# Performance work log

Hardware: AMD Instinct MI355X
Metric: run time of the kernel (lower is better)

## Reference

```python
import jax, jax.numpy as jnp
import numpy as np

B, T, D, H, DK, DV, FF = 4, 1024, 1024, 16, 64, 64, 4096


def setup_inputs() -> dict:
    key = jax.random.key(0)
    ks = jax.random.split(key, 16)
    sc = 0.02  # init scale (original uses uninitialized torch.empty; use small randn)
    n = lambda k, shape: jax.random.normal(k, shape, jnp.float32) * sc
    return dict(
        x=jax.random.normal(ks[0], (B, T, D), jnp.float32),
        y=jax.random.normal(ks[1], (B, T, D), jnp.float32),
        Wq1=n(ks[2], (H, D, DK)), Wk1=n(ks[3], (H, D, DK)),
        Wv1=n(ks[4], (H, D, DV)), Wo1=n(ks[5], (D, D)),
        Wq2=n(ks[6], (H, D, DK)), Wk2=n(ks[7], (H, D, DK)),
        Wv2=n(ks[8], (H, D, DV)), Wo2=n(ks[9], (D, D)),
        W_in=n(ks[10], (FF, D)), b_in=jnp.zeros((FF,), jnp.float32),
        W_out=n(ks[11], (D, FF)), b_out=jnp.zeros((D,), jnp.float32),
    )


def _mha(q, k, v, Wq, Wk, Wv, Wo):
    # per-head projections: (B,T,D) x (H,D,dk) -> (B,H,T,dk)
    WQ = jnp.einsum('btd,hdk->bhtk', q, Wq)
    WK = jnp.einsum('bsd,hdk->bhsk', k, Wk)
    WV = jnp.einsum('bsd,hdv->bhsv', v, Wv)
    scores = jnp.einsum('bhtk,bhsk->bhts', WQ, WK) / jnp.sqrt(jnp.float32(DK))
    # NOTE: original code softmaxes over dim=2 (the QUERY axis), kept faithfully
    attn = jax.nn.softmax(scores, axis=2)
    partial = jnp.einsum('bhts,bhsv->bhtv', attn, WV)
    partial = partial.transpose(0, 2, 1, 3).reshape(q.shape[0], q.shape[1], -1)  # (B,T,H*dv)
    return partial @ Wo


def _sub_norm(o):
    mean = o.mean(-1, keepdims=True)
    std = o.std(-1, ddof=1, keepdims=True)  # torch.std default is unbiased
    return o - mean - std  # faithful: subtract (not divide by) std


def reference(x, y, Wq1, Wk1, Wv1, Wo1, Wq2, Wk2, Wv2, Wo2, W_in, b_in, W_out, b_out):
    out1 = _sub_norm(_mha(y, y, y, Wq1, Wk1, Wv1, Wo1) + y)
    out2 = _sub_norm(_mha(y, x, x, Wq2, Wk2, Wv2, Wo2) + out1)
    ff = jax.nn.relu(y @ W_in.T + b_in) @ W_out.T + b_out  # FFN applied to y, as in source
    return _sub_norm(ff + out2)
```

## Files before the change

### kernel.cpp

```cpp
#include <hip/hip_runtime.h>


typedef unsigned short u16;
typedef __bf16 bf16x8 __attribute__((ext_vector_type(8)));
typedef float f32x4 __attribute__((ext_vector_type(4)));

__device__ __forceinline__ u16 f2bf(float f) {
    unsigned int u = __float_as_uint(f);
    u += 0x7fffu + ((u >> 16) & 1u);
    return (u16)(u >> 16);
}
__device__ __forceinline__ float bf2f(u16 b) {
    return __uint_as_float(((unsigned int)b) << 16);
}

typedef __attribute__((address_space(1))) const void* as1cv;
typedef __attribute__((address_space(3))) void* as3v;
__device__ __forceinline__ void gl_lds16(const void* g, void* l) {
    __builtin_amdgcn_global_load_lds((as1cv)g, (as3v)l, 16, 0, 0);
}

__global__ __launch_bounds__(256) void mega_pack_k(
    const float* __restrict__ yf, u16* __restrict__ yb,
    const float* __restrict__ xf, u16* __restrict__ xb,
    const float* __restrict__ W_in, u16* __restrict__ Winb,
    const float* __restrict__ W_out, u16* __restrict__ Woutb,
    const float* __restrict__ Wq1, const float* __restrict__ Wk1,
    const float* __restrict__ Wv1, const float* __restrict__ Wq2,
    u16* __restrict__ W1cat,
    const float* __restrict__ Wk2, const float* __restrict__ Wv2,
    u16* __restrict__ Wkv2t,
    const float* __restrict__ Wo1, u16* __restrict__ Wo1t,
    const float* __restrict__ Wo2, u16* __restrict__ Wo2t,
    float* __restrict__ csumz)
{
    __shared__ float tile[64][65];
    int id = blockIdx.x;
    if (id >= 18432) {
        long i = (long)(id - 18432) * 256 + threadIdx.x;
        float4 zz; zz.x = 0.f; zz.y = 0.f; zz.z = 0.f; zz.w = 0.f;
        reinterpret_cast<float4*>(csumz)[i] = zz;
        return;
    }
    if (id < 16384) {
        int j = id >> 12, local = id & 4095;
        const float* in; u16* out;
        switch (j) {
            case 0:  in = yf;    out = yb;    break;
            case 1:  in = xf;    out = xb;    break;
            case 2:  in = W_in;  out = Winb;  break;
            default: in = W_out; out = Woutb; break;
        }
        long i = (long)local * 256 + threadIdx.x;
        float4 v = reinterpret_cast<const float4*>(in)[i];
        ushort4 o;
        o.x = f2bf(v.x); o.y = f2bf(v.y); o.z = f2bf(v.z); o.w = f2bf(v.w);
        reinterpret_cast<ushort4*>(out)[i] = o;
        return;
    }
    int t = id - 16384;
    int pj = t >> 8, local = t & 255;
    const float* in; u16* out;
    int Q, R, bx, by, bz;
    if (pj < 6) {
        switch (pj) {
            case 0:  in = Wq1; out = W1cat;           break;
            case 1:  in = Wk1; out = W1cat + 1048576; break;
            case 2:  in = Wv1; out = W1cat + 2097152; break;
            case 3:  in = Wq2; out = W1cat + 3145728; break;
            case 4:  in = Wk2; out = Wkv2t;           break;
            default: in = Wv2; out = Wkv2t + 1048576; break;
        }
        Q = 1024; R = 64; bx = 0; by = local & 15; bz = local >> 4;
    } else {
        in = (pj == 6) ? Wo1 : Wo2; out = (pj == 6) ? Wo1t : Wo2t;
        Q = 1024; R = 1024; bx = local & 15; by = local >> 4; bz = 0;
    }
    int r0 = bx * 64, q0 = by * 64;
    int tx = threadIdx.x & 63, ty = threadIdx.x >> 6;
    const float* inp = in + ((long)bz * Q + q0) * R + r0;
    #pragma unroll
    for (int i = 0; i < 64; i += 4)
        tile[ty + i][tx] = inp[(long)(ty + i) * R + tx];
    __syncthreads();
    u16* outp = out + ((long)bz * R + r0) * Q + q0;
    #pragma unroll
    for (int i = 0; i < 64; i += 4)
        outp[(long)(ty + i) * Q + tx] = f2bf(tile[tx][ty + i]);
}

__global__ __launch_bounds__(256) void tscale2_k(
    const u16* __restrict__ in1, long ld1, long zs1,
    const u16* __restrict__ in2, long ld2, long zs2,
    u16* __restrict__ Vt, const float* __restrict__ csum) {
    __shared__ u16 tile[64][66];
    int z = blockIdx.z;
    int m = z >> 2, zb = z & 3;
    const u16* in; long ld, zs;
    if (m) { in = in2; ld = ld2; zs = zs2; } else { in = in1; ld = ld1; zs = zs1; }
    const u16* inz = in + (long)zb * zs;
    u16* outz = Vt + (long)m * 4194304 + (long)zb * 1048576;
    const float* cs = csum + m * 65536 + (long)zb * 16384;
    int r0 = blockIdx.y * 64;
    int c0 = blockIdx.x * 64;
    int tx = threadIdx.x & 63, ty = threadIdx.x >> 6;
    #pragma unroll
    for (int i = 0; i < 64; i += 4)
        tile[ty + i][tx] = inz[(long)(r0 + ty + i) * ld + c0 + tx];
    __syncthreads();
    #pragma unroll
    for (int i = 0; i < 64; i += 4) {
        int orow = c0 + ty + i;
        float f = bf2f(tile[tx][ty + i]) / cs[(orow >> 6) * 1024 + r0 + tx];
        outz[(long)orow * 1024 + r0 + tx] = f2bf(f);
    }
}

template<int BM, int BN, int BK, int WM, int WN, int OUT_BF16, int EPI, int SWZ, int KS, int MRG>
__global__ __launch_bounds__(256) void gemm_k(
    const u16* __restrict__ A, long lda, long a_zin, long a_zout,
    const u16* __restrict__ B, long ldb, long b_zin, long b_zout,
    void* __restrict__ Cv, long ldc, long c_zin, long c_zout,
    int zin, int K, float alpha, const float* __restrict__ bias,
    float* __restrict__ csum,
    const u16* __restrict__ A2, long lda2,
    const u16* __restrict__ B2, long ldb2, long b_zout2,
    float* __restrict__ csum2)
{
    static_assert(BK == 64, "staging assumes BK=64");
    constexpr int WTM = BM / WM;
    constexpr int WTN = BN / WN;
    constexpr int TM = WTM / 16;
    constexpr int TN = WTN / 16;
    __shared__ __align__(16) u16 smem[(BM + BN) * BK];
    u16* As = smem;
    u16* Bs = smem + BM * BK;

    int bx, by, z;
    if (SWZ == 4) {
        int L = blockIdx.x;
        if (KS > 1) { z = L >> 9; L &= 511; } else { z = 0; }
        by = (L & 7) * 4 + ((L >> 3) & 3);
        bx = L >> 5;
    } else {
        bx = blockIdx.x; by = blockIdx.y; z = blockIdx.z;
    }
    if (MRG) {
        int m2 = z >> 6; z &= 63;
        if (m2) { A = A2; lda = lda2; B = B2; ldb = ldb2; b_zout = b_zout2; csum = csum2; }
    }
    int zi = z % zin, zo = z / zin;
    A += (long)zi * a_zin + (long)zo * a_zout;
    B += (long)zi * b_zin + (long)zo * b_zout;
    long coff = (long)zi * c_zin + (long)zo * c_zout;

    int tid = threadIdx.x;
    int lane = tid & 63;
    int wave = tid >> 6;
    int wm = wave / WN, wn = wave % WN;
    long bm0 = (long)by * BM, bn0 = (long)bx * BN;

    f32x4 acc[TM][TN];
    #pragma unroll
    for (int i = 0; i < TM; ++i)
        #pragma unroll
        for (int j = 0; j < TN; ++j) {
            acc[i][j][0] = 0.f; acc[i][j][1] = 0.f;
            acc[i][j][2] = 0.f; acc[i][j][3] = 0.f;
        }

    int r16 = lane & 15;
    int quad = lane >> 4;
    int l8 = lane >> 3;
    int gsw = ((lane & 7) ^ l8) * 8;

    constexpr int ASTR = BM / 8;
    constexpr int BSTR = BN / 8;

    for (int k0 = 0; k0 < K; k0 += BK) {
        #pragma unroll
        for (int s = wave; s < ASTR; s += 4)
            gl_lds16(&A[(bm0 + s * 8 + l8) * lda + k0 + gsw], &As[s * 512]);
        #pragma unroll
        for (int s = wave; s < BSTR; s += 4)
            gl_lds16(&B[(bn0 + s * 8 + l8) * ldb + k0 + gsw], &Bs[s * 512]);
        __syncthreads();
        #pragma unroll
        for (int kk = 0; kk < BK; kk += 32) {
            int cb = (kk >> 3) + quad;
            bf16x8 av[TM], bv[TN];
            #pragma unroll
            for (int i = 0; i < TM; ++i) {
                int r = wm * WTM + i * 16 + r16;
                av[i] = *reinterpret_cast<const bf16x8*>(&As[r * 64 + ((cb ^ (r & 7)) * 8)]);
            }
            #pragma unroll
            for (int j = 0; j < TN; ++j) {
                int r = wn * WTN + j * 16 + r16;
                bv[j] = *reinterpret_cast<const bf16x8*>(&Bs[r * 64 + ((cb ^ (r & 7)) * 8)]);
            }
            #pragma unroll
            for (int i = 0; i < TM; ++i)
                #pragma unroll
                for (int j = 0; j < TN; ++j)
                    acc[i][j] = __builtin_amdgcn_mfma_f32_16x16x32_bf16(av[i], bv[j], acc[i][j], 0, 0, 0);
        }
        __syncthreads();
    }

    int rb = quad * 4;

    if (EPI == 4) {
        float csl[TN];
        #pragma unroll
        for (int j = 0; j < TN; ++j) csl[j] = 0.f;
        #pragma unroll
        for (int i = 0; i < TM; ++i)
            #pragma unroll
            for (int j = 0; j < TN; ++j)
                #pragma unroll
                for (int r = 0; r < 4; ++r)
                    csl[j] += __expf(acc[i][j][r] * alpha);
        #pragma unroll
        for (int j = 0; j < TN; ++j) {
            float cs = csl[j];
            cs += __shfl_xor(cs, 16, 64);
            cs += __shfl_xor(cs, 32, 64);
            if (quad == 0) {
                long col = bn0 + wn * WTN + j * 16 + r16;
                atomicAdd(&csum[((long)zo * zin + zi) * 1024 + col], cs);
            }
        }
        return;
    }

    constexpr int EB = OUT_BF16 ? 2 : 4;
    constexpr int CH = 16 / EB;
    constexpr int STRIDE = BN + CH;
    constexpr int LDSB = (BM + BN) * BK * 2;
    constexpr int EPASS = (BM * STRIDE * EB > LDSB) ? 2 : 1;
    constexpr int RPP = BM / EPASS;
    static_assert(RPP * STRIDE * EB <= LDSB, "epilogue tile overflows LDS");
    static_assert(EPASS == 1 || (WM == 2 && WTM == RPP), "pass/wave row alignment");
    constexpr int CPR = BN / CH;
    constexpr int NCH = RPP * CPR / 256;
    static_assert(RPP * CPR % 256 == 0, "store mapping");

    float* Ef = reinterpret_cast<float*>(smem);
    char* Cb = reinterpret_cast<char*>(Cv);

    for (int pass = 0; pass < EPASS; ++pass) {
        int p0 = pass * RPP;
        __syncthreads();
        #pragma unroll
        for (int i = 0; i < TM; ++i) {
            #pragma unroll
            for (int j = 0; j < TN; ++j) {
                int lcol = wn * WTN + j * 16 + r16;
                float bsv = (EPI == 1 || EPI == 2) ? bias[bn0 + lcol] : 0.f;
                #pragma unroll
                for (int r = 0; r < 4; ++r) {
                    int lrow = wm * WTM + i * 16 + rb + r;
                    if ((unsigned)(lrow - p0) < (unsigned)RPP) {
                        float v = acc[i][j][r] * alpha;
                        if (EPI == 1) { v += bsv; v = v > 0.f ? v : 0.f; }
                        else if (EPI == 2) { v += bsv; }
                        if (OUT_BF16) smem[(lrow - p0) * STRIDE + lcol] = f2bf(v);
                        else          Ef[(lrow - p0) * STRIDE + lcol] = v;
                    }
                }
            }
        }
        __syncthreads();
        #pragma unroll
        for (int c = 0; c < NCH; ++c) {
            int cid = tid + c * 256;
            int row = cid / CPR, ch = cid - row * CPR;
            int4 v = *reinterpret_cast<const int4*>(
                reinterpret_cast<const char*>(smem) + (row * STRIDE + ch * CH) * EB);
            long gidx = coff + (bm0 + p0 + row) * ldc + bn0 + ch * CH;
            *reinterpret_cast<int4*>(Cb + gidx * EB) = v;
        }
    }
}


__device__ __forceinline__ void bar_raw() {
    asm volatile("" ::: "memory");
    __builtin_amdgcn_s_barrier();
    asm volatile("" ::: "memory");
}

template<int N> __device__ __forceinline__ void vmw() {
    if constexpr (N == 10) asm volatile("s_waitcnt vmcnt(10)" ::: "memory");
    else if constexpr (N == 8) asm volatile("s_waitcnt vmcnt(8)" ::: "memory");
    else if constexpr (N == 4) asm volatile("s_waitcnt vmcnt(4)" ::: "memory");
    else if constexpr (N == 2) asm volatile("s_waitcnt vmcnt(2)" ::: "memory");
    else if constexpr (N == 0) asm volatile("s_waitcnt vmcnt(0)" ::: "memory");
}

__device__ __forceinline__ void stage_half(const u16* __restrict__ base, long ld, int kt,
                                           u16* __restrict__ lds, int half, int wave) {
    const u16* src = base + (long)kt * 64;
    #pragma unroll
    for (int u = 0; u < 2; ++u) {
        int s = half * 16 + u * 8 + wave;
        gl_lds16(src + (long)(s * 8) * ld, lds + s * 512);
    }
}

template<int IH>
__device__ __forceinline__ void read_a8(bf16x8 (&av)[4][2], const u16* __restrict__ As,
                                        int wm, int r16, int quad) {
    #pragma unroll
    for (int ii = 0; ii < 4; ++ii) {
        int r = IH * 128 + wm * 64 + ii * 16 + r16;
        #pragma unroll
        for (int kx = 0; kx < 2; ++kx)
            av[ii][kx] = *reinterpret_cast<const bf16x8*>(&As[r * 64 + (((kx * 4 + quad) ^ (r & 7)) * 8)]);
    }
}

template<int JH>
__device__ __forceinline__ void read_b8(bf16x8 (&bv)[2][2], const u16* __restrict__ Bs,
                                        int wn, int r16, int quad) {
    #pragma unroll
    for (int j = 0; j < 2; ++j) {
        int r = JH * 128 + wn * 32 + j * 16 + r16;
        #pragma unroll
        for (int kx = 0; kx < 2; ++kx)
            bv[j][kx] = *reinterpret_cast<const bf16x8*>(&Bs[r * 64 + (((kx * 4 + quad) ^ (r & 7)) * 8)]);
    }
}

template<int IH, int JH>
__device__ __forceinline__ void mfma_q(f32x4 (&acc)[2][4][2][2],
                                       const bf16x8 (&av)[4][2], const bf16x8 (&bv)[2][2]) {
    #pragma unroll
    for (int kx = 0; kx < 2; ++kx)
        #pragma unroll
        for (int ii = 0; ii < 4; ++ii)
            #pragma unroll
            for (int j = 0; j < 2; ++j)
                acc[IH][ii][JH][j] = __builtin_amdgcn_mfma_f32_16x16x32_bf16(
                    av[ii][kx], bv[j][kx], acc[IH][ii][JH][j], 0, 0, 0);
}

template<int MODE>
__device__ __forceinline__ void tile_iter(
    int t, f32x4 (&acc)[2][4][2][2], bf16x8 (&av)[4][2], bf16x8 (&bvh)[2][2][2],
    u16* __restrict__ smem, const u16* __restrict__ Ab, long lda,
    const u16* __restrict__ Bb, long ldb, int wave, int wm, int wn, int r16, int quad)
{
    u16* As0 = smem + (t & 1) * 32768;
    u16* Bs0 = As0 + 16384;
    u16* As1 = smem + ((t + 1) & 1) * 32768;
    read_a8<0>(av, As0, wm, r16, quad);
    read_b8<0>(bvh[0], Bs0, wn, r16, quad);
    if (MODE < 2) stage_half(Ab, lda, t + 1, As1, 1, wave);
    vmw<MODE == 0 ? 10 : (MODE == 1 ? 10 : 2)>();
    bar_raw(); __builtin_amdgcn_sched_barrier(0);
    __builtin_amdgcn_s_setprio(1);
    mfma_q<0, 0>(acc, av, bvh[0]);
    __builtin_amdgcn_s_setprio(0);
    __builtin_amdgcn_sched_barrier(0);
    bar_raw();
    read_b8<1>(bvh[1], Bs0, wn, r16, quad);
    if (MODE == 0) stage_half(Ab, lda, t + 2, As0, 0, wave);
    vmw<MODE == 0 ? 10 : (MODE == 1 ? 8 : 0)>();
    bar_raw(); __builtin_amdgcn_sched_barrier(0);
    __builtin_amdgcn_s_setprio(1);
    mfma_q<0, 1>(acc, av, bvh[1]);
    __builtin_amdgcn_s_setprio(0);
    __builtin_amdgcn_sched_barrier(0);
    bar_raw();
    read_a8<1>(av, As0, wm, r16, quad);
    if (MODE == 0) stage_half(Bb, ldb, t + 2, Bs0, 0, wave);
    bar_raw(); __builtin_amdgcn_sched_barrier(0);
    __builtin_amdgcn_s_setprio(1);
    mfma_q<1, 0>(acc, av, bvh[0]);
    __builtin_amdgcn_s_setprio(0);
    __builtin_amdgcn_sched_barrier(0);
    bar_raw();
    if (MODE == 0) stage_half(Bb, ldb, t + 2, Bs0, 1, wave);
    if (MODE < 2) vmw<MODE == 0 ? 10 : 4>();
    bar_raw(); __builtin_amdgcn_sched_barrier(0);
    __builtin_amdgcn_s_setprio(1);
    mfma_q<1, 1>(acc, av, bvh[1]);
    __builtin_amdgcn_s_setprio(0);
    __builtin_amdgcn_sched_barrier(0);
    bar_raw();
}

template<int NT, int KS, int EPI, int OUT_BF16, int SPLITN>
__global__ __launch_bounds__(512, 2) void gemm8_k(
    const u16* __restrict__ A, long lda,
    const u16* __restrict__ B, long ldb,
    void* __restrict__ Cv, void* __restrict__ Cv2, long ldc,
    int K, float alpha, const float* __restrict__ bias, long czs)
{
    __shared__ __align__(16) u16 smem[65536];

    int L = blockIdx.x;
    int z = 0;
    if (KS > 1) { z = L / (16 * NT); L -= z * 16 * NT; }
    int by = (L & 7) * 2 + ((L >> 3) & 1);
    int bx = L >> 4;
    if (KS > 1) { A += (long)z * K; B += (long)z * K; }

    int tid = threadIdx.x;
    int lane = tid & 63, wave = tid >> 6;
    int wm = wave >> 2, wn = wave & 3;
    int r16 = lane & 15, quad = lane >> 4, l8 = lane >> 3;
    int gsw = ((lane & 7) ^ l8) * 8;
    long bm0 = (long)by * 256, bn0 = (long)bx * 256;
    const u16* Ab = A + (bm0 + l8) * lda + gsw;
    const u16* Bb = B + (bn0 + l8) * ldb + gsw;

    f32x4 acc[2][4][2][2];
    #pragma unroll
    for (int a0 = 0; a0 < 2; ++a0)
        #pragma unroll
        for (int a1 = 0; a1 < 4; ++a1)
            #pragma unroll
            for (int a2 = 0; a2 < 2; ++a2)
                #pragma unroll
                for (int a3 = 0; a3 < 2; ++a3) {
                    acc[a0][a1][a2][a3][0] = 0.f; acc[a0][a1][a2][a3][1] = 0.f;
                    acc[a0][a1][a2][a3][2] = 0.f; acc[a0][a1][a2][a3][3] = 0.f;
                }
    bf16x8 av[4][2];
    bf16x8 bvh[2][2][2];

    int T = K >> 6;

    stage_half(Ab, lda, 0, smem,         0, wave);
    stage_half(Bb, ldb, 0, smem + 16384, 0, wave);
    stage_half(Bb, ldb, 0, smem + 16384, 1, wave);
    stage_half(Ab, lda, 0, smem,         1, wave);
    stage_half(Ab, lda, 1, smem + 32768, 0, wave);
    stage_half(Bb, ldb, 1, smem + 49152, 0, wave);
    stage_half(Bb, ldb, 1, smem + 49152, 1, wave);
    vmw<10>();
    bar_raw();

    for (int t = 0; t < T - 2; ++t)
        tile_iter<0>(t, acc, av, bvh, smem, Ab, lda, Bb, ldb, wave, wm, wn, r16, quad);
    tile_iter<1>(T - 2, acc, av, bvh, smem, Ab, lda, Bb, ldb, wave, wm, wn, r16, quad);
    tile_iter<2>(T - 1, acc, av, bvh, smem, Ab, lda, Bb, ldb, wave, wm, wn, r16, quad);

    constexpr int EB = OUT_BF16 ? 2 : 4;
    constexpr int EPASS = OUT_BF16 ? 1 : 2;
    bool sec = SPLITN && (bx >= NT / 2);
    char* Cb;
    long bnc = bn0;
    if (SPLITN) {
        Cb = reinterpret_cast<char*>(sec ? Cv2 : Cv);
        if (sec) bnc = bn0 - (long)(NT / 2) * 256;
    } else {
        Cb = reinterpret_cast<char*>((KS > 1 && z >= 2) ? Cv2 : Cv);
        if (KS > 1) Cb += (long)(z & 1) * czs * EB;
    }
    bool do_bias = (EPI == 1) || sec;
    float bsv[2][2];
    if (do_bias) {
        #pragma unroll
        for (int jh = 0; jh < 2; ++jh)
            #pragma unroll
            for (int j = 0; j < 2; ++j)
                bsv[jh][j] = bias[bnc + jh * 128 + wn * 32 + j * 16 + r16];
    }
    u16* sm16 = smem;
    float* smf = reinterpret_cast<float*>(smem);
    #pragma unroll
    for (int pass = 0; pass < EPASS; ++pass) {
        bar_raw();
        #pragma unroll
        for (int ih = 0; ih < 2; ++ih) {
            if (EPASS == 2 && ih != pass) continue;
            #pragma unroll
            for (int ii = 0; ii < 4; ++ii)
                #pragma unroll
                for (int jh = 0; jh < 2; ++jh)
                    #pragma unroll
                    for (int j = 0; j < 2; ++j)
                        #pragma unroll
                        for (int r = 0; r < 4; ++r) {
                            int lrow = (EPASS == 2 ? 0 : ih * 128) + wm * 64 + ii * 16 + quad * 4 + r;
                            int lcol = jh * 128 + wn * 32 + j * 16 + r16;
                            float v = acc[ih][ii][jh][j][r] * alpha;
                            if (do_bias) { v += bsv[jh][j]; v = v > 0.f ? v : 0.f; }
                            int scol = lcol ^ ((lrow & 7) * 8);
                            if (OUT_BF16) sm16[lrow * 256 + scol] = f2bf(v);
                            else          smf[lrow * 256 + scol] = v;
                        }
        }
        bar_raw();
        constexpr int CH = 16 / EB;
        constexpr int CPR = 256 / CH;
        constexpr int NCH = (OUT_BF16 ? 256 : 128) * CPR / 512;
        #pragma unroll
        for (int c = 0; c < NCH; ++c) {
            int cid = tid + c * 512;
            int row = cid / CPR, ch = cid - row * CPR;
            int col = (ch * CH) ^ ((row & 7) * 8);
            int4 v = *reinterpret_cast<const int4*>(
                reinterpret_cast<const char*>(smem) + ((long)row * 256 + col) * EB);
            long grow = bm0 + pass * 128 + row;
            *reinterpret_cast<int4*>(Cb + (grow * ldc + bnc + ch * CH) * EB) = v;
        }
    }
}

template<int MRG>
__global__ __launch_bounds__(256) void attn_pv_k(
    const u16* __restrict__ Qg, long ldq, long qbz,
    const u16* __restrict__ Kg, long ldk, long kbz,
    const u16* __restrict__ Vg, u16* __restrict__ outg,
    const u16* __restrict__ Qg2,
    const u16* __restrict__ Kg2, long ldk2, long kbz2,
    const u16* __restrict__ Vg2, u16* __restrict__ outg2)
{
    __shared__ __align__(16) u16 Qs[128 * 64];
    __shared__ __align__(16) u16 Ks[2][64 * 64];
    __shared__ __align__(16) u16 Vs[2][64 * 64];
    __shared__ __align__(16) u16 Es[128 * 64];

    int L = blockIdx.x;
    if (MRG) {
        int m = L >> 9; L &= 511;
        if (m) { Qg = Qg2; Kg = Kg2; ldk = ldk2; kbz = kbz2; Vg = Vg2; outg = outg2; }
    }
    int h  = (L & 7) * 2 + ((L >> 3) & 1);
    int tb = (L >> 4) & 7;
    int b  = L >> 7;

    const u16* Q  = Qg + (long)b * qbz + h * 64;
    const u16* Kp = Kg + (long)b * kbz + h * 64;
    const u16* Vp = Vg + (long)b * 1048576 + (long)h * 65536;
    u16* outp = outg + (long)b * 1048576 + (long)tb * 131072 + h * 64;

    int tid = threadIdx.x, lane = tid & 63, wave = tid >> 6;
    int wm = wave >> 1, wn = wave & 1;
    int r16 = lane & 15, quad = lane >> 4, l8 = lane >> 3;
    int gsw = ((lane & 7) ^ l8) * 8;
    long t0 = (long)tb * 128;

    #pragma unroll
    for (int s = wave; s < 16; s += 4)
        gl_lds16(&Q[(t0 + s * 8 + l8) * ldq + gsw], &Qs[s * 512]);
    #pragma unroll
    for (int s = wave; s < 8; s += 4) {
        gl_lds16(&Kp[(long)(s * 8 + l8) * ldk + gsw], &Ks[0][s * 512]);
        gl_lds16(&Vp[(long)(s * 8 + l8) * 1024 + gsw], &Vs[0][s * 512]);
    }

    f32x4 acc[4][2];
    #pragma unroll
    for (int i = 0; i < 4; ++i)
        #pragma unroll
        for (int j = 0; j < 2; ++j) {
            acc[i][j][0] = 0.f; acc[i][j][1] = 0.f;
            acc[i][j][2] = 0.f; acc[i][j][3] = 0.f;
        }

    for (int sc = 0; sc < 16; ++sc) {
        const u16* Ksc = Ks[sc & 1];
        const u16* Vsc = Vs[sc & 1];
        if (sc < 15) {
            int nc = sc + 1;
            u16* Kn = Ks[nc & 1];
            u16* Vn = Vs[nc & 1];
            #pragma unroll
            for (int s = wave; s < 8; s += 4) {
                gl_lds16(&Kp[(long)(nc * 64 + s * 8 + l8) * ldk + gsw], &Kn[s * 512]);
                gl_lds16(&Vp[(long)(s * 8 + l8) * 1024 + nc * 64 + gsw], &Vn[s * 512]);
            }
            asm volatile("s_waitcnt vmcnt(4)" ::: "memory");
        } else {
            asm volatile("s_waitcnt vmcnt(0)" ::: "memory");
        }
        bar_raw();

        f32x4 e[4][2];
        #pragma unroll
        for (int i = 0; i < 4; ++i)
            #pragma unroll
            for (int j = 0; j < 2; ++j) {
                e[i][j][0] = 0.f; e[i][j][1] = 0.f;
                e[i][j][2] = 0.f; e[i][j][3] = 0.f;
            }
        #pragma unroll
        for (int kk = 0; kk < 64; kk += 32) {
            int cb = (kk >> 3) + quad;
            bf16x8 av[4], bv[2];
            #pragma unroll
            for (int i = 0; i < 4; ++i) {
                int r = wm * 64 + i * 16 + r16;
                av[i] = *reinterpret_cast<const bf16x8*>(&Qs[r * 64 + ((cb ^ (r & 7)) * 8)]);
            }
            #pragma unroll
            for (int j = 0; j < 2; ++j) {
                int r = wn * 32 + j * 16 + r16;
                bv[j] = *reinterpret_cast<const bf16x8*>(&Ksc[r * 64 + ((cb ^ (r & 7)) * 8)]);
            }
            #pragma unroll
            for (int i = 0; i < 4; ++i)
                #pragma unroll
                for (int j = 0; j < 2; ++j)
                    e[i][j] = __builtin_amdgcn_mfma_f32_16x16x32_bf16(av[i], bv[j], e[i][j], 0, 0, 0);
        }
        #pragma unroll
        for (int i = 0; i < 4; ++i)
            #pragma unroll
            for (int j = 0; j < 2; ++j) {
                int lcol = wn * 32 + j * 16 + r16;
                #pragma unroll
                for (int r = 0; r < 4; ++r) {
                    int lrow = wm * 64 + i * 16 + quad * 4 + r;
                    float v = __expf(e[i][j][r] * 0.125f);
                    Es[lrow * 64 + (((lcol >> 3) ^ (lrow & 7)) * 8) + (lcol & 7)] = f2bf(v);
                }
            }
        asm volatile("s_waitcnt lgkmcnt(0)" ::: "memory");
        bar_raw();

        #pragma unroll
        for (int kk = 0; kk < 64; kk += 32) {
            int cb = (kk >> 3) + quad;
            bf16x8 av[4], bv[2];
            #pragma unroll
            for (int i = 0; i < 4; ++i) {
                int r = wm * 64 + i * 16 + r16;
                av[i] = *reinterpret_cast<const bf16x8*>(&Es[r * 64 + ((cb ^ (r & 7)) * 8)]);
            }
            #pragma unroll
            for (int j = 0; j < 2; ++j) {
                int r = wn * 32 + j * 16 + r16;
                bv[j] = *reinterpret_cast<const bf16x8*>(&Vsc[r * 64 + ((cb ^ (r & 7)) * 8)]);
            }
            #pragma unroll
            for (int i = 0; i < 4; ++i)
                #pragma unroll
                for (int j = 0; j < 2; ++j)
                    acc[i][j] = __builtin_amdgcn_mfma_f32_16x16x32_bf16(av[i], bv[j], acc[i][j], 0, 0, 0);
        }
        bar_raw();
    }

    #pragma unroll
    for (int i = 0; i < 4; ++i)
        #pragma unroll
        for (int j = 0; j < 2; ++j) {
            int lcol = wn * 32 + j * 16 + r16;
            #pragma unroll
            for (int r = 0; r < 4; ++r) {
                int lrow = wm * 64 + i * 16 + quad * 4 + r;
                outp[(long)lrow * 1024 + lcol] = f2bf(acc[i][j][r]);
            }
        }
}

template<int NP, int BIAS>
__global__ __launch_bounds__(256) void addsn_k(const float* __restrict__ parts,
                                               const float* __restrict__ parts2,
                                               long pstride,
                                               const float* __restrict__ resid,
                                               const float* __restrict__ bias,
                                               float* __restrict__ out) {
    __shared__ float sm[8];
    long row = blockIdx.x;
    int tid = threadIdx.x;
    float4 x = reinterpret_cast<const float4*>(resid + row * 1024)[tid];
    #pragma unroll
    for (int p = 0; p < NP; ++p) {
        const float* src = (p < 2) ? (parts + p * pstride) : (parts2 + (p - 2) * pstride);
        float4 a = reinterpret_cast<const float4*>(src + row * 1024)[tid];
        x.x += a.x; x.y += a.y; x.z += a.z; x.w += a.w;
    }
    if (BIAS) {
        float4 bb = reinterpret_cast<const float4*>(bias)[tid];
        x.x += bb.x; x.y += bb.y; x.z += bb.z; x.w += bb.w;
    }
    float s = x.x + x.y + x.z + x.w;
    for (int o = 32; o > 0; o >>= 1) s += __shfl_down(s, o, 64);
    int lane = tid & 63, w = tid >> 6;
    if (lane == 0) sm[w] = s;
    __syncthreads();
    float mean = (sm[0] + sm[1] + sm[2] + sm[3]) * (1.f / 1024.f);
    float d0 = x.x - mean, d1 = x.y - mean, d2 = x.z - mean, d3 = x.w - mean;
    float q = d0 * d0 + d1 * d1 + d2 * d2 + d3 * d3;
    for (int o = 32; o > 0; o >>= 1) q += __shfl_down(q, o, 64);
    if (lane == 0) sm[w + 4] = q;
    __syncthreads();
    float sd = sqrtf((sm[4] + sm[5] + sm[6] + sm[7]) * (1.f / 1023.f));
    float4 ov;
    ov.x = d0 - sd; ov.y = d1 - sd; ov.z = d2 - sd; ov.w = d3 - sd;
    reinterpret_cast<float4*>(out + row * 1024)[tid] = ov;
}


extern "C" void kernel_launch(void* const* d_in, const int* in_sizes, int n_in,
                              void* d_out, int out_size, void* d_ws, size_t ws_size,
                              hipStream_t stream) {
    (void)in_sizes; (void)n_in; (void)out_size; (void)ws_size;
    const float* xf   = (const float*)d_in[0];
    const float* yf   = (const float*)d_in[1];
    const float* Wq1  = (const float*)d_in[2];
    const float* Wk1  = (const float*)d_in[3];
    const float* Wv1  = (const float*)d_in[4];
    const float* Wo1  = (const float*)d_in[5];
    const float* Wq2  = (const float*)d_in[6];
    const float* Wk2  = (const float*)d_in[7];
    const float* Wv2  = (const float*)d_in[8];
    const float* Wo2  = (const float*)d_in[9];
    const float* W_in = (const float*)d_in[10];
    const float* b_in = (const float*)d_in[11];
    const float* W_out= (const float*)d_in[12];
    const float* b_out= (const float*)d_in[13];

    char* p = (char*)d_ws;
    auto alloc = [&](size_t bytes) { char* r = p; p += bytes; return r; };
    u16*   yb    = (u16*)alloc(8388608);
    u16*   xb    = (u16*)alloc(8388608);
    u16*   W1cat = (u16*)alloc(8388608);
    u16*   Winb  = (u16*)alloc(8388608);
    u16*   Wkv2t = (u16*)alloc(4194304);
    u16*   Wo1t  = (u16*)alloc(2097152);
    u16*   Wo2t  = (u16*)alloc(2097152);
    u16*   Woutb = (u16*)alloc(8388608);
    u16*   QKV   = (u16*)alloc(33554432);
    u16*   KV2   = (u16*)alloc(16777216);
    u16*   Pb    = (u16*)alloc(33554432);
    u16*   part  = (u16*)alloc(16777216);
    float* gout  = (float*)alloc(33554432);
    u16*   Vt    = yb;
    float* csum  = gout;
    float* out1  = (float*)part;
    float* ffnC2 = (float*)yb;

    mega_pack_k<<<18560, 256, 0, stream>>>(
        yf, yb, xf, xb, W_in, Winb, W_out, Woutb,
        Wq1, Wk1, Wv1, Wq2, W1cat, Wk2, Wv2, Wkv2t,
        Wo1, Wo1t, Wo2, Wo2t, csum);

    gemm8_k<32,1,0,1,1><<<512, 512, 0, stream>>>(
        yb, 1024L, W1cat, 1024L, (void*)QKV, (void*)Pb, 4096L, 1024, 1.0f, b_in, 0L);
    gemm8_k<8,1,0,1,0><<<128, 512, 0, stream>>>(
        xb, 1024L, Wkv2t, 1024L, (void*)KV2, nullptr, 2048L, 1024, 1.0f, nullptr, 0L);

    gemm_k<128,128,64,2,2,1,4,0,1,1><<<dim3(8, 8, 128), 256, 0, stream>>>(
        QKV, 4096L, 64L, 4194304L,
        QKV + 1024, 4096L, 64L, 4194304L,
        (void*)Pb, 1024L, 0L, 0L, 16, 64, 0.125f, nullptr, csum,
        QKV + 3072, 4096L,
        KV2, 2048L, 2097152L,
        csum + 65536);

    tscale2_k<<<dim3(16, 16, 8), 256, 0, stream>>>(
        QKV + 2048, 4096L, 4194304L,
        KV2 + 1024, 2048L, 2097152L,
        Vt, csum);

    attn_pv_k<1><<<1024, 256, 0, stream>>>(
        QKV, 4096L, 4194304L, QKV + 1024, 4096L, 4194304L, Vt, part,
        QKV + 3072, KV2, 2048L, 2097152L, Vt + 4194304, part + 4194304);

    gemm_k<128,64,64,2,2,0,0,4,2,0><<<1024, 256, 0, stream>>>(
        part, 1024L, 0L, 4194304L, Wo1t, 1024L, 0L, 1048576L,
        (void*)gout, 1024L, 0L, 4194304L, 1, 1024, 1.0f, nullptr, nullptr,
        nullptr, 0L, nullptr, 0L, 0L, nullptr);

    gemm8_k<4,4,0,0,0><<<256, 512, 0, stream>>>(
        Pb, 4096L, Woutb, 4096L, (void*)QKV, (void*)ffnC2, 1024L, 1024, 1.0f, nullptr, 4194304L);

    addsn_k<1,0><<<4096, 256, 0, stream>>>(gout, nullptr, 0L, yf, nullptr, out1);
    addsn_k<1,0><<<4096, 256, 0, stream>>>(gout + 4194304, nullptr, 0L, out1, nullptr, (float*)d_out);
    addsn_k<4,1><<<4096, 256, 0, stream>>>((const float*)QKV, ffnC2, 4194304L,
                                           (const float*)d_out, b_out, (float*)d_out);
}
```

Baseline: 481.7 us.

## Fuse three add-subnorm passes into one kernel and retile KV2 projection GEMM

```diff
diff --git a/kernel.cpp b/kernel.cpp
--- a/kernel.cpp
+++ b/kernel.cpp
@@ -661,42 +661,53 @@
         }
 }
 
-template<int NP, int BIAS>
-__global__ __launch_bounds__(256) void addsn_k(const float* __restrict__ parts,
-                                               const float* __restrict__ parts2,
-                                               long pstride,
-                                               const float* __restrict__ resid,
-                                               const float* __restrict__ bias,
-                                               float* __restrict__ out) {
+__global__ __launch_bounds__(256) void addsn_fuse_k(
+    const float* __restrict__ g0, const float* __restrict__ g1,
+    const float* __restrict__ f01, const float* __restrict__ f23, long fstride,
+    const float* __restrict__ yf, const float* __restrict__ b_out,
+    float* __restrict__ out)
+{
     __shared__ float sm[8];
     long row = blockIdx.x;
     int tid = threadIdx.x;
-    float4 x = reinterpret_cast<const float4*>(resid + row * 1024)[tid];
-    #pragma unroll
-    for (int p = 0; p < NP; ++p) {
-        const float* src = (p < 2) ? (parts + p * pstride) : (parts2 + (p - 2) * pstride);
-        float4 a = reinterpret_cast<const float4*>(src + row * 1024)[tid];
-        x.x += a.x; x.y += a.y; x.z += a.z; x.w += a.w;
-    }
-    if (BIAS) {
-        float4 bb = reinterpret_cast<const float4*>(bias)[tid];
-        x.x += bb.x; x.y += bb.y; x.z += bb.z; x.w += bb.w;
-    }
-    float s = x.x + x.y + x.z + x.w;
-    for (int o = 32; o > 0; o >>= 1) s += __shfl_down(s, o, 64);
     int lane = tid & 63, w = tid >> 6;
-    if (lane == 0) sm[w] = s;
-    __syncthreads();
-    float mean = (sm[0] + sm[1] + sm[2] + sm[3]) * (1.f / 1024.f);
-    float d0 = x.x - mean, d1 = x.y - mean, d2 = x.z - mean, d3 = x.w - mean;
-    float q = d0 * d0 + d1 * d1 + d2 * d2 + d3 * d3;
-    for (int o = 32; o > 0; o >>= 1) q += __shfl_down(q, o, 64);
-    if (lane == 0) sm[w + 4] = q;
-    __syncthreads();
-    float sd = sqrtf((sm[4] + sm[5] + sm[6] + sm[7]) * (1.f / 1023.f));
-    float4 ov;
-    ov.x = d0 - sd; ov.y = d1 - sd; ov.z = d2 - sd; ov.w = d3 - sd;
-    reinterpret_cast<float4*>(out + row * 1024)[tid] = ov;
+
+    auto subnorm = [&](float4& x) {
+        float s = x.x + x.y + x.z + x.w;
+        for (int o = 32; o > 0; o >>= 1) s += __shfl_down(s, o, 64);
+        if (lane == 0) sm[w] = s;
+        __syncthreads();
+        float mean = (sm[0] + sm[1] + sm[2] + sm[3]) * (1.f / 1024.f);
+        float d0 = x.x - mean, d1 = x.y - mean, d2 = x.z - mean, d3 = x.w - mean;
+        float q = d0 * d0 + d1 * d1 + d2 * d2 + d3 * d3;
+        for (int o = 32; o > 0; o >>= 1) q += __shfl_down(q, o, 64);
+        if (lane == 0) sm[w + 4] = q;
+        __syncthreads();
+        float sd = sqrtf((sm[4] + sm[5] + sm[6] + sm[7]) * (1.f / 1023.f));
+        x.x = d0 - sd; x.y = d1 - sd; x.z = d2 - sd; x.w = d3 - sd;
+    };
+
+    float4 x = reinterpret_cast<const float4*>(yf + row * 1024)[tid];
+    float4 a = reinterpret_cast<const float4*>(g0 + row * 1024)[tid];
+    x.x += a.x; x.y += a.y; x.z += a.z; x.w += a.w;
+    subnorm(x);
+
+    a = reinterpret_cast<const float4*>(g1 + row * 1024)[tid];
+    x.x += a.x; x.y += a.y; x.z += a.z; x.w += a.w;
+    subnorm(x);
+
+    float4 f0 = reinterpret_cast<const float4*>(f01 + row * 1024)[tid];
+    float4 f1 = reinterpret_cast<const float4*>(f01 + fstride + row * 1024)[tid];
+    float4 f2 = reinterpret_cast<const float4*>(f23 + row * 1024)[tid];
+    float4 f3 = reinterpret_cast<const float4*>(f23 + fstride + row * 1024)[tid];
+    float4 bb = reinterpret_cast<const float4*>(b_out)[tid];
+    x.x += f0.x + f1.x + f2.x + f3.x + bb.x;
+    x.y += f0.y + f1.y + f2.y + f3.y + bb.y;
+    x.z += f0.z + f1.z + f2.z + f3.z + bb.z;
+    x.w += f0.w + f1.w + f2.w + f3.w + bb.w;
+    subnorm(x);
+
+    reinterpret_cast<float4*>(out + row * 1024)[tid] = x;
 }
 
 
@@ -736,7 +747,6 @@
     float* gout  = (float*)alloc(33554432);
     u16*   Vt    = yb;
     float* csum  = gout;
-    float* out1  = (float*)part;
     float* ffnC2 = (float*)yb;
 
     mega_pack_k<<<18560, 256, 0, stream>>>(
@@ -746,8 +756,11 @@
 
     gemm8_k<32,1,0,1,1><<<512, 512, 0, stream>>>(
         yb, 1024L, W1cat, 1024L, (void*)QKV, (void*)Pb, 4096L, 1024, 1.0f, b_in, 0L);
-    gemm8_k<8,1,0,1,0><<<128, 512, 0, stream>>>(
-        xb, 1024L, Wkv2t, 1024L, (void*)KV2, nullptr, 2048L, 1024, 1.0f, nullptr, 0L);
+
+    gemm_k<128,128,64,2,2,1,0,0,1,0><<<dim3(16, 32, 1), 256, 0, stream>>>(
+        xb, 1024L, 0L, 0L, Wkv2t, 1024L, 0L, 0L,
+        (void*)KV2, 2048L, 0L, 0L, 1, 1024, 1.0f, nullptr, nullptr,
+        nullptr, 0L, nullptr, 0L, 0L, nullptr);
 
     gemm_k<128,128,64,2,2,1,4,0,1,1><<<dim3(8, 8, 128), 256, 0, stream>>>(
         QKV, 4096L, 64L, 4194304L,
@@ -774,8 +787,7 @@
     gemm8_k<4,4,0,0,0><<<256, 512, 0, stream>>>(
         Pb, 4096L, Woutb, 4096L, (void*)QKV, (void*)ffnC2, 1024L, 1024, 1.0f, nullptr, 4194304L);
 
-    addsn_k<1,0><<<4096, 256, 0, stream>>>(gout, nullptr, 0L, yf, nullptr, out1);
-    addsn_k<1,0><<<4096, 256, 0, stream>>>(gout + 4194304, nullptr, 0L, out1, nullptr, (float*)d_out);
-    addsn_k<4,1><<<4096, 256, 0, stream>>>((const float*)QKV, ffnC2, 4194304L,
-                                           (const float*)d_out, b_out, (float*)d_out);
-}
+    addsn_fuse_k<<<4096, 256, 0, stream>>>(
+        gout, gout + 4194304, (const float*)QKV, ffnC2, 4194304L,
+        yf, b_out, (float*)d_out);
+}
```

Result: faster. 470.7 us (-2.3%).
